# Optimization experiments

Measured on AMD Instinct MI355X. Metric: run time of the kernel, lower is better.

The kernel has to match this reference:

```python
import jax, jax.numpy as jnp
import numpy as np

B, S, H = 16, 512, 768
NH, DH = 12, 64  # heads, head dim (H = NH*DH)
E = 8            # number of experts


def setup_inputs() -> dict:
    key = jax.random.key(0)
    ks = jax.random.split(key, 9)
    w_scale = 1.0 / np.sqrt(H).astype(np.float32)
    return {
        "hidden_states": jax.random.normal(ks[0], (B, S, H), jnp.float32),
        "attention_mask": jnp.zeros((B, 1, 1, S), jnp.float32),
        "Wq": jax.random.normal(ks[1], (E, H, H), jnp.float32) * w_scale,
        "bq": jnp.zeros((E, H), jnp.float32),
        "Wk": jax.random.normal(ks[2], (E, H, H), jnp.float32) * w_scale,
        "bk": jnp.zeros((E, H), jnp.float32),
        "Wv": jax.random.normal(ks[3], (E, H, H), jnp.float32) * w_scale,
        "bv": jnp.zeros((E, H), jnp.float32),
        "expert_idx": jax.random.randint(ks[4], (B,), 0, E, jnp.int64),
    }


def reference(hidden_states, attention_mask, Wq, bq, Wk, bk, Wv, bv, expert_idx):
    b, s, h = hidden_states.shape

    def proj(W, bias):
        # Per-sample expert selection: math-equivalent to computing all experts
        # then slice_for_expert, but gathers weights instead of activations.
        Wg = W[expert_idx]            # [B, H_out, H_in]
        bg = bias[expert_idx]         # [B, H_out]
        y = jnp.einsum('bsd,bod->bso', hidden_states, Wg) + bg[:, None, :]
        return y.reshape(b, s, NH, DH).transpose(0, 2, 1, 3)  # [B, NH, S, DH]

    q = proj(Wq, bq)
    k = proj(Wk, bk)
    v = proj(Wv, bv)

    scores = jnp.einsum('bhqd,bhkd->bhqk', q, k) / np.sqrt(DH).astype(np.float32)
    scores = scores + attention_mask
    probs = jax.nn.softmax(scores, axis=-1)  # dropout p=0.0 (eval)
    ctx = jnp.einsum('bhqk,bhkd->bhqd', probs, v)
    return ctx.transpose(0, 2, 1, 3).reshape(b, s, h)
```

## Files before the change

### kernel.cpp

```cpp
#include <hip/hip_runtime.h>
#include <hip/hip_bf16.h>
#include <stdint.h>

typedef __bf16 bf16;
typedef bf16 bf16x8 __attribute__((ext_vector_type(8)));
typedef bf16 bf16x4 __attribute__((ext_vector_type(4)));
typedef float f32x4 __attribute__((ext_vector_type(4)));

#define MFMA_16x16x32(a, b, c) __builtin_amdgcn_mfma_f32_16x16x32_bf16((a), (b), (c), 0, 0, 0)

constexpr int B = 16, S = 512, H = 768, NH = 12, DH = 64;
constexpr long NHID = (long)B * S * H;
constexpr long NW = (long)8 * H * H;

constexpr size_t XB_OFF = 0;
constexpr size_t XB_SZ  = (size_t)NHID * 2;
constexpr size_t W_SZ   = (size_t)NW * 2;
constexpr size_t WQ_OFF = XB_OFF + XB_SZ;
constexpr size_t WK_OFF = WQ_OFF + W_SZ;
constexpr size_t WV_OFF = WK_OFF + W_SZ;
constexpr size_t PROJ_SZ = (size_t)B * NH * S * DH * 2;
constexpr size_t QB_OFF = WV_OFF + W_SZ;
constexpr size_t KB_OFF = QB_OFF + PROJ_SZ;
constexpr size_t VB_OFF = KB_OFF + PROJ_SZ;
constexpr size_t WS_NEED = VB_OFF + PROJ_SZ;

__global__ void cvt_all(const float* __restrict__ x,
                        const float* __restrict__ wq, const float* __restrict__ wk,
                        const float* __restrict__ wv,
                        bf16* __restrict__ xb, bf16* __restrict__ wqb,
                        bf16* __restrict__ wkb, bf16* __restrict__ wvb) {
  long i = ((long)blockIdx.x * blockDim.x + threadIdx.x) * 8;
  const float* src;
  bf16* dst;
  long off;
  if (i < NHID)               { src = x;  dst = xb;  off = i; }
  else if (i < NHID + NW)     { src = wq; dst = wqb; off = i - NHID; }
  else if (i < NHID + 2 * NW) { src = wk; dst = wkb; off = i - NHID - NW; }
  else if (i < NHID + 3 * NW) { src = wv; dst = wvb; off = i - NHID - 2 * NW; }
  else return;
  const float4* sp = reinterpret_cast<const float4*>(src + off);
  float4 a = sp[0], b = sp[1];
  bf16x8 o;
  o[0] = (bf16)a.x; o[1] = (bf16)a.y; o[2] = (bf16)a.z; o[3] = (bf16)a.w;
  o[4] = (bf16)b.x; o[5] = (bf16)b.y; o[6] = (bf16)b.z; o[7] = (bf16)b.w;
  *reinterpret_cast<bf16x8*>(dst + off) = o;
}

__global__ __launch_bounds__(512, 2) void proj_gemm(
    const bf16* __restrict__ Xb,
    const bf16* __restrict__ Wqb, const bf16* __restrict__ Wkb, const bf16* __restrict__ Wvb,
    const float* __restrict__ bq, const float* __restrict__ bk, const float* __restrict__ bv,
    const int* __restrict__ eidx,
    bf16* __restrict__ Qb, bf16* __restrict__ Kb, bf16* __restrict__ Vb)
{
  __shared__ __align__(16) char smem[73728];
  bf16* Asb = (bf16*)smem;
  bf16* Bsb = (bf16*)(smem + 32768);

  const int xcd = blockIdx.x & 7;
  const int bi  = blockIdx.x >> 3;
  const int b   = xcd * 2 + (bi / 36);
  const int rem = bi % 36;
  const int m0  = (rem / 18) * 256;
  const int gy  = rem % 18;
  const int proj = gy / 6;
  const int n0 = (gy % 6) * 128;
  const int e = eidx[b];

  const bf16* W = (proj == 0 ? Wqb : (proj == 1 ? Wkb : Wvb)) + (size_t)e * H * H;
  const float* bias = (proj == 0 ? bq : (proj == 1 ? bk : bv)) + (size_t)e * H;
  bf16* Out = (proj == 0 ? Qb : (proj == 1 ? Kb : Vb));

  const int tid = threadIdx.x;
  const int lane = tid & 63;
  const int wave = tid >> 6;
  const int wm = wave >> 1, wn = wave & 1;
  const int r = lane & 15, lg = lane >> 4;

  const bf16* Abase = Xb + ((size_t)b * S + m0) * H;
  const bf16* Bbase = W + (size_t)n0 * H;

  const int srow = lane >> 2;
  const int sg = ((lane & 3) ^ ((lane >> 3) & 3)) * 8;

  auto stage = [&](int kt, int pb) {
    const int k0 = kt * 32;
#pragma unroll
    for (int i = 0; i < 2; ++i) {
      const int seg = wave * 2 + i;
      const bf16* ga = Abase + (size_t)(seg * 16 + srow) * H + k0 + sg;
      __builtin_amdgcn_global_load_lds(
          (const __attribute__((address_space(1))) void*)ga,
          (__attribute__((address_space(3))) void*)(&Asb[pb * 8192 + seg * 512]), 16, 0, 0);
    }
    const bf16* gb = Bbase + (size_t)(wave * 16 + srow) * H + k0 + sg;
    __builtin_amdgcn_global_load_lds(
        (const __attribute__((address_space(1))) void*)gb,
        (__attribute__((address_space(3))) void*)(&Bsb[pb * 4096 + wave * 512]), 16, 0, 0);
  };

  f32x4 acc[4][4] = {};

  stage(0, 0);
  __syncthreads();

  const int sz = (r >> 1) & 3;

  int buf = 0;
#pragma unroll 1
  for (int kt = 0; kt < 24; ++kt) {
    if (kt < 23) stage(kt + 1, buf ^ 1);

    bf16x8 af[4], bfr[4];
#pragma unroll
    for (int mi = 0; mi < 4; ++mi)
      af[mi] = *reinterpret_cast<const bf16x8*>(
          &Asb[buf * 8192 + (wm * 64 + mi * 16 + r) * 32 + ((lg ^ sz) * 8)]);
#pragma unroll
    for (int ni = 0; ni < 4; ++ni)
      bfr[ni] = *reinterpret_cast<const bf16x8*>(
          &Bsb[buf * 4096 + (wn * 64 + ni * 16 + r) * 32 + ((lg ^ sz) * 8)]);
#pragma unroll
    for (int mi = 0; mi < 4; ++mi)
#pragma unroll
      for (int ni = 0; ni < 4; ++ni)
        acc[mi][ni] = MFMA_16x16x32(af[mi], bfr[ni], acc[mi][ni]);

    __syncthreads();
    buf ^= 1;
  }

  if (proj != 2) {
    bf16* ep = (bf16*)smem + wave * 4352;
#pragma unroll
    for (int ni = 0; ni < 4; ++ni) {
      const int col = ni * 16 + r;
      const float bb = bias[n0 + wn * 64 + col];
#pragma unroll
      for (int mi = 0; mi < 4; ++mi)
#pragma unroll
        for (int rr = 0; rr < 4; ++rr)
          ep[(mi * 16 + lg * 4 + rr) * 68 + col] = (bf16)(acc[mi][ni][rr] + bb);
    }
    const int nh = (n0 + wn * 64) >> 6;
    bf16* gb = Out + (((size_t)b * NH + nh) * S + (m0 + wm * 64)) * DH;
    const int sub = lane & 7, rowL = lane >> 3;
#pragma unroll
    for (int pass = 0; pass < 8; ++pass) {
      const int row = pass * 8 + rowL;
      bf16x8 v = *reinterpret_cast<const bf16x8*>(&ep[row * 68 + sub * 8]);
      *reinterpret_cast<bf16x8*>(&gb[(size_t)row * DH + sub * 8]) = v;
    }
  } else {
#pragma unroll
    for (int ni = 0; ni < 4; ++ni) {
      const int col = n0 + wn * 64 + ni * 16 + r;
      const int nh = col >> 6, dh = col & 63;
      const float bb = bias[col];
      bf16* orow = Out + ((size_t)b * NH + nh) * DH * S + (size_t)dh * S;
#pragma unroll
      for (int mi = 0; mi < 4; ++mi) {
        bf16x4 v;
#pragma unroll
        for (int rr = 0; rr < 4; ++rr) v[rr] = (bf16)(acc[mi][ni][rr] + bb);
        *reinterpret_cast<bf16x4*>(orow + m0 + wm * 64 + mi * 16 + lg * 4) = v;
      }
    }
  }
}

__global__ __launch_bounds__(256, 3) void attn_kernel(
    const bf16* __restrict__ Qb, const bf16* __restrict__ Kb, const bf16* __restrict__ VTb,
    const float* __restrict__ mask, float* __restrict__ out)
{
  __shared__ __align__(16) bf16 Ks[2][64 * 64];
  __shared__ __align__(16) bf16 Vs[2][64 * 64];
  __shared__ float maskS[512];

  const int x = blockIdx.x;
  const int xcd = x & 7;
  const int grp = x >> 3;
  const int qblk = grp & 3;
  const int bh = (grp >> 2) * 8 + xcd;
  const int b = bh / NH;
  const int h = bh % NH;
  const int tid = threadIdx.x;
  const int wave = tid >> 6;
  const int lane = tid & 63;
  const int r = lane & 15, lg = lane >> 4;
  const int qbase = qblk * 128 + wave * 32;

  const bf16* Q  = Qb  + (size_t)bh * S * DH;
  const bf16* K  = Kb  + (size_t)bh * S * DH;
  const bf16* VT = VTb + (size_t)bh * DH * S;

  for (int i = tid; i < S; i += 256) maskS[i] = mask[b * S + i];

  const int srowoff = lane >> 3;
  const int sg = (lane & 7) ^ srowoff;

  auto stage = [&](int kt, int buf) {
    const int kb = kt * 64;
#pragma unroll
    for (int i = 0; i < 2; ++i) {
      const int c = wave * 2 + i;
      const int row = c * 8 + srowoff;
      const bf16* gk = K + (size_t)(kb + row) * DH + sg * 8;
      __builtin_amdgcn_global_load_lds(
          (const __attribute__((address_space(1))) void*)gk,
          (__attribute__((address_space(3))) void*)(&Ks[buf][c * 512]), 16, 0, 0);
      const bf16* gv = VT + (size_t)row * S + kb + sg * 8;
      __builtin_amdgcn_global_load_lds(
          (const __attribute__((address_space(1))) void*)gv,
          (__attribute__((address_space(3))) void*)(&Vs[buf][c * 512]), 16, 0, 0);
    }
  };

  bf16x8 qf0[2], qf1[2];
#pragma unroll
  for (int g = 0; g < 2; ++g) {
    const bf16* qr = &Q[(size_t)(qbase + g * 16 + r) * DH];
    qf0[g] = *reinterpret_cast<const bf16x8*>(qr + lg * 8);
    qf1[g] = *reinterpret_cast<const bf16x8*>(qr + 32 + lg * 8);
  }

  stage(0, 0);
  __syncthreads();

  float mr[2] = {-3.0e38f, -3.0e38f};
  float lr[2] = {0.f, 0.f};
  f32x4 ctx[2][4] = {};
  int buf = 0;

#pragma unroll 1
  for (int kt = 0; kt < 8; ++kt) {
    const int kb = kt * 64;
    if (kt < 7) stage(kt + 1, buf ^ 1);

    f32x4 sa[2][4];
#pragma unroll
    for (int t = 0; t < 4; ++t) {
      const int row = t * 16 + r;
      const int sw = row & 7;
      bf16x8 kf0 = *reinterpret_cast<const bf16x8*>(&Ks[buf][row * 64 + ((lg ^ sw) * 8)]);
      bf16x8 kf1 = *reinterpret_cast<const bf16x8*>(&Ks[buf][row * 64 + (((lg + 4) ^ sw) * 8)]);
#pragma unroll
      for (int g = 0; g < 2; ++g) {
        f32x4 a = {};
        a = MFMA_16x16x32(kf0, qf0[g], a);
        a = MFMA_16x16x32(kf1, qf1[g], a);
        sa[g][t] = a;
      }
    }

#pragma unroll
    for (int g = 0; g < 2; ++g) {
      float tmax = -3.0e38f;
#pragma unroll
      for (int t = 0; t < 4; ++t)
#pragma unroll
        for (int rr = 0; rr < 4; ++rr) {
          float s = sa[g][t][rr] * 0.125f + maskS[kb + t * 16 + lg * 4 + rr];
          sa[g][t][rr] = s;
          tmax = fmaxf(tmax, s);
        }
      tmax = fmaxf(tmax, __shfl_xor(tmax, 16));
      tmax = fmaxf(tmax, __shfl_xor(tmax, 32));
      const float mnew = fmaxf(mr[g], tmax);
      const float scale = __expf(mr[g] - mnew);
      mr[g] = mnew;
      float ps = 0.f;
#pragma unroll
      for (int t = 0; t < 4; ++t)
#pragma unroll
        for (int rr = 0; rr < 4; ++rr) {
          float p = __expf(sa[g][t][rr] - mnew);
          sa[g][t][rr] = p;
          ps += p;
        }
      lr[g] = lr[g] * scale + ps;
#pragma unroll
      for (int dt = 0; dt < 4; ++dt) ctx[g][dt] *= scale;
    }

#pragma unroll
    for (int kc = 0; kc < 2; ++kc) {
      bf16x8 pf[2];
#pragma unroll
      for (int g = 0; g < 2; ++g) {
        f32x4 p0 = sa[g][2 * kc], p1 = sa[g][2 * kc + 1];
        bf16x8 o;
        o[0] = (bf16)p0[0]; o[1] = (bf16)p0[1]; o[2] = (bf16)p0[2]; o[3] = (bf16)p0[3];
        o[4] = (bf16)p1[0]; o[5] = (bf16)p1[1]; o[6] = (bf16)p1[2]; o[7] = (bf16)p1[3];
        pf[g] = o;
      }
      const int chunk_lo = kc * 4 + (lg >> 1);
      const int rem = (lg & 1) * 4;
#pragma unroll
      for (int dt = 0; dt < 4; ++dt) {
        const int row = dt * 16 + r;
        const int sw = row & 7;
        const bf16* vlo = &Vs[buf][row * 64 + ((chunk_lo ^ sw) * 8) + rem];
        const bf16* vhi = &Vs[buf][row * 64 + (((chunk_lo + 2) ^ sw) * 8) + rem];
        bf16x4 lo = *reinterpret_cast<const bf16x4*>(vlo);
        bf16x4 hi = *reinterpret_cast<const bf16x4*>(vhi);
        bf16x8 vf;
        vf[0] = lo[0]; vf[1] = lo[1]; vf[2] = lo[2]; vf[3] = lo[3];
        vf[4] = hi[0]; vf[5] = hi[1]; vf[6] = hi[2]; vf[7] = hi[3];
#pragma unroll
        for (int g = 0; g < 2; ++g)
          ctx[g][dt] = MFMA_16x16x32(vf, pf[g], ctx[g][dt]);
      }
    }

    __syncthreads();
    buf ^= 1;
  }

#pragma unroll
  for (int g = 0; g < 2; ++g) {
    float l = lr[g];
    l += __shfl_xor(l, 16);
    l += __shfl_xor(l, 32);
    const float inv = 1.0f / l;
    float* obase = out + ((size_t)b * S + qbase + g * 16 + r) * H + h * DH;
#pragma unroll
    for (int dt = 0; dt < 4; ++dt) {
      float4 o;
      o.x = ctx[g][dt][0] * inv; o.y = ctx[g][dt][1] * inv;
      o.z = ctx[g][dt][2] * inv; o.w = ctx[g][dt][3] * inv;
      *reinterpret_cast<float4*>(obase + dt * 16 + lg * 4) = o;
    }
  }
}

extern "C" void kernel_launch(void* const* d_in, const int* in_sizes, int n_in,
                              void* d_out, int out_size, void* d_ws, size_t ws_size,
                              hipStream_t stream) {
  const float* hidden = (const float*)d_in[0];
  const float* mask   = (const float*)d_in[1];
  const float* Wq = (const float*)d_in[2];
  const float* bq = (const float*)d_in[3];
  const float* Wk = (const float*)d_in[4];
  const float* bk = (const float*)d_in[5];
  const float* Wv = (const float*)d_in[6];
  const float* bv = (const float*)d_in[7];
  const int* eidx = (const int*)d_in[8];

  if (ws_size < WS_NEED) return;

  char* ws = (char*)d_ws;
  bf16* Xb  = (bf16*)(ws + XB_OFF);
  bf16* Wqb = (bf16*)(ws + WQ_OFF);
  bf16* Wkb = (bf16*)(ws + WK_OFF);
  bf16* Wvb = (bf16*)(ws + WV_OFF);
  bf16* Qbf = (bf16*)(ws + QB_OFF);
  bf16* Kbf = (bf16*)(ws + KB_OFF);
  bf16* Vbf = (bf16*)(ws + VB_OFF);
  float* out = (float*)d_out;

  cvt_all<<<9984, 256, 0, stream>>>(hidden, Wq, Wk, Wv, Xb, Wqb, Wkb, Wvb);
  proj_gemm<<<576, 512, 0, stream>>>(Xb, Wqb, Wkb, Wvb, bq, bk, bv, eidx,
                                     Qbf, Kbf, Vbf);
  attn_kernel<<<768, 256, 0, stream>>>(Qbf, Kbf, Vbf, mask, out);
}
```

Measured before the change: 96.94 us.

## Retile projection GEMM to 128x192, fold Q scaling, lazy softmax rescale

The projection GEMM tile changes from 256x128 to 128x192, so 768 blocks launch instead of 576 and less LDS is used, aiming at better CU fill across the GPU. The 1/sqrt(DH) scale moves into the Q projection epilogue, which removes one multiply per score in attention. The online softmax now rescales the running max, sum and context only when a new tile's max exceeds the old max by more than 6, skipping the exp and scaling work in most iterations. Keeping a stale max means the exponentials can exceed 1 by up to about e^6, which trims bf16 headroom.

```diff
diff --git a/kernel.cpp b/kernel.cpp
--- a/kernel.cpp
+++ b/kernel.cpp
@@ -54,28 +54,29 @@
     const int* __restrict__ eidx,
     bf16* __restrict__ Qb, bf16* __restrict__ Kb, bf16* __restrict__ Vb)
 {
-  __shared__ __align__(16) char smem[73728];
+  __shared__ __align__(16) char smem[57344];
   bf16* Asb = (bf16*)smem;
-  bf16* Bsb = (bf16*)(smem + 32768);
+  bf16* Bsb = (bf16*)(smem + 16384);
 
   const int xcd = blockIdx.x & 7;
   const int bi  = blockIdx.x >> 3;
-  const int b   = xcd * 2 + (bi / 36);
-  const int rem = bi % 36;
-  const int m0  = (rem / 18) * 256;
-  const int gy  = rem % 18;
-  const int proj = gy / 6;
-  const int n0 = (gy % 6) * 128;
+  const int b   = xcd * 2 + (bi / 48);
+  const int rem = bi % 48;
+  const int proj = rem / 16;
+  const int t16 = rem % 16;
+  const int m0  = (t16 >> 2) * 128;
+  const int n0  = (t16 & 3) * 192;
   const int e = eidx[b];
 
   const bf16* W = (proj == 0 ? Wqb : (proj == 1 ? Wkb : Wvb)) + (size_t)e * H * H;
   const float* bias = (proj == 0 ? bq : (proj == 1 ? bk : bv)) + (size_t)e * H;
   bf16* Out = (proj == 0 ? Qb : (proj == 1 ? Kb : Vb));
+  const float oscale = (proj == 0) ? 0.125f : 1.0f;
 
   const int tid = threadIdx.x;
   const int lane = tid & 63;
   const int wave = tid >> 6;
-  const int wm = wave >> 1, wn = wave & 1;
+  const int wm = wave >> 2, wn = wave & 3;
   const int r = lane & 15, lg = lane >> 4;
 
   const bf16* Abase = Xb + ((size_t)b * S + m0) * H;
@@ -86,21 +87,23 @@
 
   auto stage = [&](int kt, int pb) {
     const int k0 = kt * 32;
-#pragma unroll
-    for (int i = 0; i < 2; ++i) {
-      const int seg = wave * 2 + i;
-      const bf16* ga = Abase + (size_t)(seg * 16 + srow) * H + k0 + sg;
+    const bf16* ga = Abase + (size_t)(wave * 16 + srow) * H + k0 + sg;
+    __builtin_amdgcn_global_load_lds(
+        (const __attribute__((address_space(1))) void*)ga,
+        (__attribute__((address_space(3))) void*)(&Asb[pb * 4096 + wave * 512]), 16, 0, 0);
+    const bf16* gb0 = Bbase + (size_t)(wave * 16 + srow) * H + k0 + sg;
+    __builtin_amdgcn_global_load_lds(
+        (const __attribute__((address_space(1))) void*)gb0,
+        (__attribute__((address_space(3))) void*)(&Bsb[pb * 6144 + wave * 512]), 16, 0, 0);
+    if (wave < 4) {
+      const bf16* gb1 = Bbase + (size_t)((8 + wave) * 16 + srow) * H + k0 + sg;
       __builtin_amdgcn_global_load_lds(
-          (const __attribute__((address_space(1))) void*)ga,
-          (__attribute__((address_space(3))) void*)(&Asb[pb * 8192 + seg * 512]), 16, 0, 0);
-    }
-    const bf16* gb = Bbase + (size_t)(wave * 16 + srow) * H + k0 + sg;
-    __builtin_amdgcn_global_load_lds(
-        (const __attribute__((address_space(1))) void*)gb,
-        (__attribute__((address_space(3))) void*)(&Bsb[pb * 4096 + wave * 512]), 16, 0, 0);
+          (const __attribute__((address_space(1))) void*)gb1,
+          (__attribute__((address_space(3))) void*)(&Bsb[pb * 6144 + (8 + wave) * 512]), 16, 0, 0);
+    }
   };
 
-  f32x4 acc[4][4] = {};
+  f32x4 acc[4][3] = {};
 
   stage(0, 0);
   __syncthreads();
@@ -112,19 +115,19 @@
   for (int kt = 0; kt < 24; ++kt) {
     if (kt < 23) stage(kt + 1, buf ^ 1);
 
-    bf16x8 af[4], bfr[4];
+    bf16x8 af[4], bfr[3];
 #pragma unroll
     for (int mi = 0; mi < 4; ++mi)
       af[mi] = *reinterpret_cast<const bf16x8*>(
-          &Asb[buf * 8192 + (wm * 64 + mi * 16 + r) * 32 + ((lg ^ sz) * 8)]);
-#pragma unroll
-    for (int ni = 0; ni < 4; ++ni)
+          &Asb[buf * 4096 + (wm * 64 + mi * 16 + r) * 32 + ((lg ^ sz) * 8)]);
+#pragma unroll
+    for (int ni = 0; ni < 3; ++ni)
       bfr[ni] = *reinterpret_cast<const bf16x8*>(
-          &Bsb[buf * 4096 + (wn * 64 + ni * 16 + r) * 32 + ((lg ^ sz) * 8)]);
+          &Bsb[buf * 6144 + (wn * 48 + ni * 16 + r) * 32 + ((lg ^ sz) * 8)]);
 #pragma unroll
     for (int mi = 0; mi < 4; ++mi)
 #pragma unroll
-      for (int ni = 0; ni < 4; ++ni)
+      for (int ni = 0; ni < 3; ++ni)
         acc[mi][ni] = MFMA_16x16x32(af[mi], bfr[ni], acc[mi][ni]);
 
     __syncthreads();
@@ -132,30 +135,33 @@
   }
 
   if (proj != 2) {
-    bf16* ep = (bf16*)smem + wave * 4352;
-#pragma unroll
-    for (int ni = 0; ni < 4; ++ni) {
+    bf16* ep = (bf16*)smem + wave * 3584;
+#pragma unroll
+    for (int ni = 0; ni < 3; ++ni) {
       const int col = ni * 16 + r;
-      const float bb = bias[n0 + wn * 64 + col];
+      const float bb = bias[n0 + wn * 48 + col];
 #pragma unroll
       for (int mi = 0; mi < 4; ++mi)
 #pragma unroll
         for (int rr = 0; rr < 4; ++rr)
-          ep[(mi * 16 + lg * 4 + rr) * 68 + col] = (bf16)(acc[mi][ni][rr] + bb);
-    }
-    const int nh = (n0 + wn * 64) >> 6;
-    bf16* gb = Out + (((size_t)b * NH + nh) * S + (m0 + wm * 64)) * DH;
-    const int sub = lane & 7, rowL = lane >> 3;
-#pragma unroll
-    for (int pass = 0; pass < 8; ++pass) {
-      const int row = pass * 8 + rowL;
-      bf16x8 v = *reinterpret_cast<const bf16x8*>(&ep[row * 68 + sub * 8]);
-      *reinterpret_cast<bf16x8*>(&gb[(size_t)row * DH + sub * 8]) = v;
+          ep[(mi * 16 + lg * 4 + rr) * 56 + col] = (bf16)((acc[mi][ni][rr] + bb) * oscale);
+    }
+    const int rowL = lane >> 3, sub = lane & 7;
+    if (sub < 6) {
+      const int gcol = n0 + wn * 48 + sub * 8;
+      const int nh = gcol >> 6, dh = gcol & 63;
+      bf16* gdst = Out + (((size_t)b * NH + nh) * S + m0 + wm * 64) * DH + dh;
+#pragma unroll
+      for (int pass = 0; pass < 8; ++pass) {
+        const int row = pass * 8 + rowL;
+        bf16x8 v = *reinterpret_cast<const bf16x8*>(&ep[row * 56 + sub * 8]);
+        *reinterpret_cast<bf16x8*>(&gdst[(size_t)row * DH]) = v;
+      }
     }
   } else {
 #pragma unroll
-    for (int ni = 0; ni < 4; ++ni) {
-      const int col = n0 + wn * 64 + ni * 16 + r;
+    for (int ni = 0; ni < 3; ++ni) {
+      const int col = n0 + wn * 48 + ni * 16 + r;
       const int nh = col >> 6, dh = col & 63;
       const float bb = bias[col];
       bf16* orow = Out + ((size_t)b * NH + nh) * DH * S + (size_t)dh * S;
@@ -261,27 +267,30 @@
       for (int t = 0; t < 4; ++t)
 #pragma unroll
         for (int rr = 0; rr < 4; ++rr) {
-          float s = sa[g][t][rr] * 0.125f + maskS[kb + t * 16 + lg * 4 + rr];
+          float s = sa[g][t][rr] + maskS[kb + t * 16 + lg * 4 + rr];
           sa[g][t][rr] = s;
           tmax = fmaxf(tmax, s);
         }
       tmax = fmaxf(tmax, __shfl_xor(tmax, 16));
       tmax = fmaxf(tmax, __shfl_xor(tmax, 32));
-      const float mnew = fmaxf(mr[g], tmax);
-      const float scale = __expf(mr[g] - mnew);
-      mr[g] = mnew;
+      if (!__all(tmax <= mr[g] + 6.0f)) {
+        const float mnew = fmaxf(mr[g], tmax);
+        const float scale = __expf(mr[g] - mnew);
+        lr[g] *= scale;
+#pragma unroll
+        for (int dt = 0; dt < 4; ++dt) ctx[g][dt] *= scale;
+        mr[g] = mnew;
+      }
       float ps = 0.f;
 #pragma unroll
       for (int t = 0; t < 4; ++t)
 #pragma unroll
         for (int rr = 0; rr < 4; ++rr) {
-          float p = __expf(sa[g][t][rr] - mnew);
+          float p = __expf(sa[g][t][rr] - mr[g]);
           sa[g][t][rr] = p;
           ps += p;
         }
-      lr[g] = lr[g] * scale + ps;
-#pragma unroll
-      for (int dt = 0; dt < 4; ++dt) ctx[g][dt] *= scale;
+      lr[g] += ps;
     }
 
 #pragma unroll
@@ -361,7 +370,7 @@
   float* out = (float*)d_out;
 
   cvt_all<<<9984, 256, 0, stream>>>(hidden, Wq, Wk, Wv, Xb, Wqb, Wkb, Wvb);
-  proj_gemm<<<576, 512, 0, stream>>>(Xb, Wqb, Wkb, Wvb, bq, bk, bv, eidx,
+  proj_gemm<<<768, 512, 0, stream>>>(Xb, Wqb, Wkb, Wvb, bq, bk, bv, eidx,
                                      Qbf, Kbf, Vbf);
   attn_kernel<<<768, 256, 0, stream>>>(Qbf, Kbf, Vbf, mask, out);
 }
```

Result: faster. 89.43 us (-7.7%).
